# Performance work log

Hardware: AMD Instinct MI355X
Metric: run time of the kernel (lower is better)

Reference implementation:

```python
import jax, jax.numpy as jnp
import numpy as np

BITS = 4
GROUP = 128
IN = 4096
OUT = 14336
B = 64
PACK = 32 // BITS          # 8 values per int32
MAXQ = (1 << BITS) - 1     # 15


def setup_inputs() -> dict:
    key = jax.random.key(0)
    k = jax.random.split(key, 5)
    x = jax.random.normal(k[0], (B, IN), dtype=jnp.float32)
    # non-negative int32 so arithmetic right-shift behaves like logical shift
    qweight = jax.random.randint(k[1], (IN // PACK, OUT), 0, 2**31 - 1, dtype=jnp.int32)
    qzeros = jax.random.randint(k[2], (IN // GROUP, OUT // PACK), 0, 2**31 - 1, dtype=jnp.int32)
    scales = jax.random.uniform(k[3], (IN // GROUP, OUT), dtype=jnp.float32,
                                minval=1e-3, maxval=1e-2)
    bias = jax.random.normal(k[4], (OUT,), dtype=jnp.float32) * 0.01
    g_idx = (jnp.arange(IN) // GROUP).astype(jnp.int32)
    return dict(x=x, qweight=qweight, qzeros=qzeros, scales=scales, bias=bias, g_idx=g_idx)


def _dequant(qweight, qzeros, scales, g_idx):
    shifts = jnp.arange(PACK, dtype=jnp.int32) * BITS  # [PACK]
    # unpack weights: [IN//PACK, PACK, OUT] -> [IN, OUT]
    w = (qweight[:, None, :] >> shifts[None, :, None]) & MAXQ
    w = w.reshape(IN, OUT)
    # unpack zeros: [G, OUT//PACK, PACK] -> [G, OUT]; pack() stored (zeros-1), so add 1 back
    z = (qzeros[:, :, None] >> shifts[None, None, :]) & MAXQ
    z = z.reshape(-1, OUT) + 1
    # per-group dequant with arbitrary g_idx (act-order support)
    return scales[g_idx] * (w - z[g_idx]).astype(scales.dtype)


def reference(x, qweight, qzeros, scales, bias, g_idx):
    W = _dequant(qweight, qzeros, scales, g_idx)  # [IN, OUT]
    return x @ W + bias
```

## Files before the change

### kernel.cpp

```cpp
#include <hip/hip_runtime.h>
#include <hip/hip_bf16.h>

using u32 = unsigned int;
using u16 = unsigned short;

typedef __attribute__((ext_vector_type(8))) _Float16 half8;
typedef __attribute__((ext_vector_type(2))) _Float16 half2v;
typedef __attribute__((ext_vector_type(16))) float f32x16;
typedef __attribute__((ext_vector_type(4))) u32 u32x4;

#define IN_K   4096
#define OUT_N  14336
#define SPLITK 8
#define OUT_ELEMS (64 * OUT_N)

__global__ __launch_bounds__(256) void prep_kernel(const float* __restrict__ x,
                                                   u16* __restrict__ xs) {
  const int t = blockIdx.x * 256 + threadIdx.x;
  const int c = t >> 6;
  const int r = t & 63;
  const float* px = x + r * IN_K + c * 8;
  const float4 a = *(const float4*)px;
  const float4 b = *(const float4*)(px + 4);
  const float af[4] = {a.x, a.y, a.z, a.w};
  const float bf[4] = {b.x, b.y, b.z, b.w};
  union { u32x4 v; u32 u[4]; } o;
#pragma unroll
  for (int i = 0; i < 4; ++i) {
    const _Float16 hl = (_Float16)af[i];
    const _Float16 hh = (_Float16)bf[i];
    u16 lo, hi;
    __builtin_memcpy(&lo, &hl, 2);
    __builtin_memcpy(&hi, &hh, 2);
    o.u[i] = (u32)lo | ((u32)hi << 16);
  }
  *(u32x4*)(xs + (size_t)t * 8) = o.v;
}

__global__ __launch_bounds__(256) void bias_init_kernel(const float* __restrict__ bias,
                                                        float* __restrict__ out) {
  const int i = (blockIdx.x * 256 + threadIdx.x) * 4;
  const int col = i % OUT_N;
  *(float4*)(out + i) = *(const float4*)(bias + col);
}

__global__ __launch_bounds__(256) void reduce_kernel(const float* __restrict__ part,
                                                     const float* __restrict__ bias,
                                                     float* __restrict__ out) {
  const int gx = blockIdx.x, ry = blockIdx.y, t = threadIdx.x;
  const int bx = gx >> 1, half = gx & 1;
  const int row = ry * 8 + (t >> 5);
  const int cin = half * 128 + (t & 31) * 4;
  const float* p = part + (((size_t)bx * SPLITK) * 64 + row) * 256 + cin;
  float4 r = *(const float4*)(bias + bx * 256 + cin);
#pragma unroll
  for (int by = 0; by < SPLITK; ++by) {
    const float4 a = *(const float4*)(p + (size_t)by * 64 * 256);
    r.x += a.x; r.y += a.y; r.z += a.z; r.w += a.w;
  }
  *(float4*)(out + (size_t)row * OUT_N + bx * 256 + cin) = r;
}

static __device__ __forceinline__ half8 dequant8(u32 q, half2v hz, half2v s2) {
  const u32 p0 = (q & 0x000F000Fu) | 0x64006400u;
  const u32 p1 = ((q >> 4) & 0x000F000Fu) | 0x64006400u;
  const u32 p2 = ((q >> 8) & 0x000F000Fu) | 0x64006400u;
  const u32 p3 = ((q >> 12) & 0x000F000Fu) | 0x64006400u;
  half2v t0, t1, t2, t3;
  __builtin_memcpy(&t0, &p0, 4);
  __builtin_memcpy(&t1, &p1, 4);
  __builtin_memcpy(&t2, &p2, 4);
  __builtin_memcpy(&t3, &p3, 4);
  union { half8 v; half2v h[4]; } bb;
  bb.h[0] = (t0 - hz) * s2;
  bb.h[1] = (t1 - hz) * s2;
  bb.h[2] = (t2 - hz) * s2;
  bb.h[3] = (t3 - hz) * s2;
  return bb.v;
}

template <bool ATOMIC>
__global__ __launch_bounds__(512, 4) void qgemm_kernel(
    const u32* __restrict__ qw, const u32* __restrict__ qz,
    const float* __restrict__ scal, const u16* __restrict__ xs,
    float* __restrict__ dst) {
  __shared__ u16 alds[64 * 512];
  const int tid = threadIdx.x;
  const int lane = tid & 63;
  const int wv = tid >> 6;
  const int g = lane >> 5;
  const int nn = lane & 31;
  const int bx = blockIdx.x;
  const int by = blockIdx.y;
  const int colabs = bx * 256 + wv * 32 + nn;
  const int chunk0 = by * 64;
  const int grp0 = by * 4;
  const int zsh = (nn & 7) * 4;

  f32x16 acc0, acc1;
#pragma unroll
  for (int i = 0; i < 16; ++i) { acc0[i] = 0.f; acc1[i] = 0.f; }

  const u16* asrc = xs + (size_t)chunk0 * 512;
#pragma unroll
  for (int r = 0; r < 8; ++r) {
    const int p = r * 512 + tid;
    __builtin_amdgcn_global_load_lds(
        (const __attribute__((address_space(1))) void*)(asrc + p * 8),
        (__attribute__((address_space(3))) void*)(&alds[0] + p * 8), 16, 0, 0);
  }

  const u32* pq = qw + (size_t)(chunk0 + g) * OUT_N + colabs;
  u32 qv[32];
#pragma unroll
  for (int i = 0; i < 32; ++i) qv[i] = pq[(size_t)(2 * i) * OUT_N];

  float sv[4]; u32 zv[4];
#pragma unroll
  for (int t = 0; t < 4; ++t) {
    sv[t] = scal[(size_t)(grp0 + t) * OUT_N + colabs];
    zv[t] = qz[(size_t)(grp0 + t) * (OUT_N / 8) + (colabs >> 3)];
  }

  asm volatile("s_waitcnt vmcnt(0)" ::: "memory");
  __builtin_amdgcn_s_barrier();
  asm volatile("" ::: "memory");

#pragma unroll
  for (int grp = 0; grp < 4; ++grp) {
    const u32 zq = (zv[grp] >> zsh) & 0xFu;
    const u32 hzu = 0x64016401u + zq * 0x00010001u;
    half2v hz; __builtin_memcpy(&hz, &hzu, 4);
    const _Float16 hs = (_Float16)sv[grp];
    const half2v s2 = {hs, hs};
#pragma unroll
    for (int s = 0; s < 8; ++s) {
      const int t = grp * 8 + s;
      const int cl = 2 * t + g;
      const half8 a0 = *(const half8*)(&alds[0] + ((size_t)cl * 64 + nn) * 8);
      const half8 a1 = *(const half8*)(&alds[0] + ((size_t)cl * 64 + nn + 32) * 8);
      const half8 bb = dequant8(qv[t], hz, s2);
      acc0 = __builtin_amdgcn_mfma_f32_32x32x16_f16(a0, bb, acc0, 0, 0, 0);
      acc1 = __builtin_amdgcn_mfma_f32_32x32x16_f16(a1, bb, acc1, 0, 0, 0);
    }
  }

  if (ATOMIC) {
#pragma unroll
    for (int r = 0; r < 16; ++r) {
      const int row = (r & 3) + 8 * (r >> 2) + 4 * g;
      unsafeAtomicAdd(&dst[(size_t)row * OUT_N + colabs], acc0[r]);
      unsafeAtomicAdd(&dst[(size_t)(row + 32) * OUT_N + colabs], acc1[r]);
    }
  } else {
    float* p = dst + (((size_t)bx * SPLITK + by) * 64) * 256 + wv * 32 + nn;
#pragma unroll
    for (int r = 0; r < 16; ++r) {
      const int row = (r & 3) + 8 * (r >> 2) + 4 * g;
      p[(size_t)row * 256] = acc0[r];
      p[(size_t)(row + 32) * 256] = acc1[r];
    }
  }
}

extern "C" void kernel_launch(void* const* d_in, const int* in_sizes, int n_in,
                              void* d_out, int out_size, void* d_ws, size_t ws_size,
                              hipStream_t stream) {
  (void)in_sizes; (void)n_in; (void)out_size;
  const float* x    = (const float*)d_in[0];
  const u32*   qw   = (const u32*)d_in[1];
  const u32*   qz   = (const u32*)d_in[2];
  const float* sc   = (const float*)d_in[3];
  const float* bias = (const float*)d_in[4];
  float* out = (float*)d_out;

  const size_t XS_BYTES   = (size_t)64 * IN_K * 2;
  const size_t PART_BYTES = (size_t)56 * SPLITK * 64 * 256 * 4;
  u16* xs = (u16*)d_ws;

  prep_kernel<<<128, 256, 0, stream>>>(x, xs);

  if (ws_size >= XS_BYTES + PART_BYTES) {
    float* part = (float*)((char*)d_ws + XS_BYTES);
    qgemm_kernel<false><<<dim3(56, SPLITK), 512, 0, stream>>>(qw, qz, sc, xs, part);
    reduce_kernel<<<dim3(112, 8), 256, 0, stream>>>(part, bias, out);
  } else {
    bias_init_kernel<<<896, 256, 0, stream>>>(bias, out);
    qgemm_kernel<true><<<dim3(56, SPLITK), 512, 0, stream>>>(qw, qz, sc, xs, out);
  }
}
```

Baseline: 32.35 us.

## Move split-K reduction into block with double-buffered LDS pipeline, drop reduce kernel

Replaces the 56x8 split-K grid plus separate reduce kernel with 224 blocks that each cover 64 output columns. The four wave pairs in a block each take a quarter of K and combine their partial sums through shared memory in the epilogue, which also adds the bias. Activations and packed weights are streamed through double-buffered LDS using global_load_lds, with waitcnt and barriers so loads overlap the MFMA work. This removes the partials buffer round trip through global memory and one kernel launch. In exchange each block uses 80KB of LDS, needs many barriers, and the grid is smaller.

Result: faster. 26.36 us (-18.5%).

```diff
diff --git a/kernel.cpp b/kernel.cpp
--- a/kernel.cpp
+++ b/kernel.cpp
@@ -11,8 +11,7 @@
 
 #define IN_K   4096
 #define OUT_N  14336
-#define SPLITK 8
-#define OUT_ELEMS (64 * OUT_N)
+#define NST    16
 
 __global__ __launch_bounds__(256) void prep_kernel(const float* __restrict__ x,
                                                    u16* __restrict__ xs) {
@@ -37,30 +36,6 @@
   *(u32x4*)(xs + (size_t)t * 8) = o.v;
 }
 
-__global__ __launch_bounds__(256) void bias_init_kernel(const float* __restrict__ bias,
-                                                        float* __restrict__ out) {
-  const int i = (blockIdx.x * 256 + threadIdx.x) * 4;
-  const int col = i % OUT_N;
-  *(float4*)(out + i) = *(const float4*)(bias + col);
-}
-
-__global__ __launch_bounds__(256) void reduce_kernel(const float* __restrict__ part,
-                                                     const float* __restrict__ bias,
-                                                     float* __restrict__ out) {
-  const int gx = blockIdx.x, ry = blockIdx.y, t = threadIdx.x;
-  const int bx = gx >> 1, half = gx & 1;
-  const int row = ry * 8 + (t >> 5);
-  const int cin = half * 128 + (t & 31) * 4;
-  const float* p = part + (((size_t)bx * SPLITK) * 64 + row) * 256 + cin;
-  float4 r = *(const float4*)(bias + bx * 256 + cin);
-#pragma unroll
-  for (int by = 0; by < SPLITK; ++by) {
-    const float4 a = *(const float4*)(p + (size_t)by * 64 * 256);
-    r.x += a.x; r.y += a.y; r.z += a.z; r.w += a.w;
-  }
-  *(float4*)(out + (size_t)row * OUT_N + bx * 256 + cin) = r;
-}
-
 static __device__ __forceinline__ half8 dequant8(u32 q, half2v hz, half2v s2) {
   const u32 p0 = (q & 0x000F000Fu) | 0x64006400u;
   const u32 p1 = ((q >> 4) & 0x000F000Fu) | 0x64006400u;
@@ -79,113 +54,135 @@
   return bb.v;
 }
 
-template <bool ATOMIC>
 __global__ __launch_bounds__(512, 4) void qgemm_kernel(
     const u32* __restrict__ qw, const u32* __restrict__ qz,
     const float* __restrict__ scal, const u16* __restrict__ xs,
-    float* __restrict__ dst) {
-  __shared__ u16 alds[64 * 512];
+    const float* __restrict__ bias, float* __restrict__ out) {
+  __shared__ alignas(16) char smem[81920];
   const int tid = threadIdx.x;
   const int lane = tid & 63;
-  const int wv = tid >> 6;
   const int g = lane >> 5;
   const int nn = lane & 31;
+  const int wv = tid >> 6;
+  const int ch = wv & 1;
+  const int kq = wv >> 1;
+  const int tq = tid & 127;
   const int bx = blockIdx.x;
-  const int by = blockIdx.y;
-  const int colabs = bx * 256 + wv * 32 + nn;
-  const int chunk0 = by * 64;
-  const int grp0 = by * 4;
+  const int colabs = bx * 64 + ch * 32 + nn;
   const int zsh = (nn & 7) * 4;
+  char* const base = smem + kq * 20480;
 
   f32x16 acc0, acc1;
 #pragma unroll
   for (int i = 0; i < 16; ++i) { acc0[i] = 0.f; acc1[i] = 0.f; }
 
-  const u16* asrc = xs + (size_t)chunk0 * 512;
+  float sv[8]; u32 zv[8];
 #pragma unroll
-  for (int r = 0; r < 8; ++r) {
-    const int p = r * 512 + tid;
+  for (int t = 0; t < 8; ++t) {
+    sv[t] = scal[(size_t)(kq * 8 + t) * OUT_N + colabs];
+    zv[t] = qz[(size_t)(kq * 8 + t) * (OUT_N / 8) + (colabs >> 3)];
+  }
+  asm volatile("s_waitcnt vmcnt(0)" ::: "memory");
+
+  auto issue = [&](int st) {
+    const int slot = st & 1;
+    char* ab = base + slot * 8192;
+    char* qb = base + 16384 + slot * 2048;
+    const u16* asrc = xs + (size_t)(kq * 128 + st * 8) * 512;
+#pragma unroll
+    for (int r = 0; r < 4; ++r) {
+      const int p = r * 128 + tq;
+      __builtin_amdgcn_global_load_lds(
+          (const __attribute__((address_space(1))) void*)(asrc + p * 8),
+          (__attribute__((address_space(3))) void*)(ab + p * 16), 16, 0, 0);
+    }
+    const int j = tq >> 4, cg = tq & 15;
+    const u32* qsrc = qw + (size_t)(kq * 128 + st * 8 + j) * OUT_N
+                         + bx * 64 + cg * 4;
     __builtin_amdgcn_global_load_lds(
-        (const __attribute__((address_space(1))) void*)(asrc + p * 8),
-        (__attribute__((address_space(3))) void*)(&alds[0] + p * 8), 16, 0, 0);
-  }
+        (const __attribute__((address_space(1))) void*)qsrc,
+        (__attribute__((address_space(3))) void*)(qb + tq * 16), 16, 0, 0);
+  };
 
-  const u32* pq = qw + (size_t)(chunk0 + g) * OUT_N + colabs;
-  u32 qv[32];
-#pragma unroll
-  for (int i = 0; i < 32; ++i) qv[i] = pq[(size_t)(2 * i) * OUT_N];
-
-  float sv[4]; u32 zv[4];
-#pragma unroll
-  for (int t = 0; t < 4; ++t) {
-    sv[t] = scal[(size_t)(grp0 + t) * OUT_N + colabs];
-    zv[t] = qz[(size_t)(grp0 + t) * (OUT_N / 8) + (colabs >> 3)];
-  }
-
-  asm volatile("s_waitcnt vmcnt(0)" ::: "memory");
-  __builtin_amdgcn_s_barrier();
-  asm volatile("" ::: "memory");
+  issue(0); issue(1);
 
 #pragma unroll
-  for (int grp = 0; grp < 4; ++grp) {
-    const u32 zq = (zv[grp] >> zsh) & 0xFu;
+  for (int st = 0; st < NST; ++st) {
+    if (st < NST - 1)
+      asm volatile("s_waitcnt vmcnt(5)" ::: "memory");
+    else
+      asm volatile("s_waitcnt vmcnt(0)" ::: "memory");
+    __builtin_amdgcn_s_barrier();
+    asm volatile("" ::: "memory");
+
+    const int gi = st >> 1;
+    const u32 zq = (zv[gi] >> zsh) & 0xFu;
     const u32 hzu = 0x64016401u + zq * 0x00010001u;
     half2v hz; __builtin_memcpy(&hz, &hzu, 4);
-    const _Float16 hs = (_Float16)sv[grp];
+    const _Float16 hs = (_Float16)sv[gi];
     const half2v s2 = {hs, hs};
+
+    const u16* ab = (const u16*)(base + (st & 1) * 8192);
+    const u32* qb = (const u32*)(base + 16384 + (st & 1) * 2048);
+    __builtin_amdgcn_s_setprio(1);
 #pragma unroll
-    for (int s = 0; s < 8; ++s) {
-      const int t = grp * 8 + s;
-      const int cl = 2 * t + g;
-      const half8 a0 = *(const half8*)(&alds[0] + ((size_t)cl * 64 + nn) * 8);
-      const half8 a1 = *(const half8*)(&alds[0] + ((size_t)cl * 64 + nn + 32) * 8);
-      const half8 bb = dequant8(qv[t], hz, s2);
+    for (int s = 0; s < 4; ++s) {
+      const int cl = s * 2 + g;
+      const half8 a0 = *(const half8*)(ab + (cl * 64 + nn) * 8);
+      const half8 a1 = *(const half8*)(ab + (cl * 64 + nn + 32) * 8);
+      const u32 q = qb[cl * 64 + ch * 32 + nn];
+      const half8 bb = dequant8(q, hz, s2);
       acc0 = __builtin_amdgcn_mfma_f32_32x32x16_f16(a0, bb, acc0, 0, 0, 0);
       acc1 = __builtin_amdgcn_mfma_f32_32x32x16_f16(a1, bb, acc1, 0, 0, 0);
     }
+    __builtin_amdgcn_s_setprio(0);
+
+    if (st + 2 < NST) {
+      __builtin_amdgcn_s_barrier();
+      asm volatile("" ::: "memory");
+      issue(st + 2);
+    }
   }
 
-  if (ATOMIC) {
+  __syncthreads();
+  float* ep = (float*)smem + kq * 4096;
 #pragma unroll
-    for (int r = 0; r < 16; ++r) {
-      const int row = (r & 3) + 8 * (r >> 2) + 4 * g;
-      unsafeAtomicAdd(&dst[(size_t)row * OUT_N + colabs], acc0[r]);
-      unsafeAtomicAdd(&dst[(size_t)(row + 32) * OUT_N + colabs], acc1[r]);
-    }
-  } else {
-    float* p = dst + (((size_t)bx * SPLITK + by) * 64) * 256 + wv * 32 + nn;
+  for (int r = 0; r < 16; ++r) {
+    const int row0 = (r & 3) + 8 * (r >> 2) + 4 * g;
+    ep[row0 * 64 + ch * 32 + nn] = acc0[r];
+    ep[(row0 + 32) * 64 + ch * 32 + nn] = acc1[r];
+  }
+  __syncthreads();
+  const int pos = tid * 8;
+  const int row = pos >> 6;
+  const int colb = pos & 63;
+  const float* eb = (const float*)smem;
+  float4 v0 = *(const float4*)(bias + bx * 64 + colb);
+  float4 v1 = *(const float4*)(bias + bx * 64 + colb + 4);
 #pragma unroll
-    for (int r = 0; r < 16; ++r) {
-      const int row = (r & 3) + 8 * (r >> 2) + 4 * g;
-      p[(size_t)row * 256] = acc0[r];
-      p[(size_t)(row + 32) * 256] = acc1[r];
-    }
+  for (int q = 0; q < 4; ++q) {
+    const float4 a = *(const float4*)(eb + q * 4096 + pos);
+    const float4 b = *(const float4*)(eb + q * 4096 + pos + 4);
+    v0.x += a.x; v0.y += a.y; v0.z += a.z; v0.w += a.w;
+    v1.x += b.x; v1.y += b.y; v1.z += b.z; v1.w += b.w;
   }
+  float* po = out + (size_t)row * OUT_N + bx * 64 + colb;
+  *(float4*)po = v0;
+  *(float4*)(po + 4) = v1;
 }
 
 extern "C" void kernel_launch(void* const* d_in, const int* in_sizes, int n_in,
                               void* d_out, int out_size, void* d_ws, size_t ws_size,
                               hipStream_t stream) {
-  (void)in_sizes; (void)n_in; (void)out_size;
+  (void)in_sizes; (void)n_in; (void)out_size; (void)ws_size;
   const float* x    = (const float*)d_in[0];
   const u32*   qw   = (const u32*)d_in[1];
   const u32*   qz   = (const u32*)d_in[2];
   const float* sc   = (const float*)d_in[3];
   const float* bias = (const float*)d_in[4];
   float* out = (float*)d_out;
-
-  const size_t XS_BYTES   = (size_t)64 * IN_K * 2;
-  const size_t PART_BYTES = (size_t)56 * SPLITK * 64 * 256 * 4;
   u16* xs = (u16*)d_ws;
 
   prep_kernel<<<128, 256, 0, stream>>>(x, xs);
-
-  if (ws_size >= XS_BYTES + PART_BYTES) {
-    float* part = (float*)((char*)d_ws + XS_BYTES);
-    qgemm_kernel<false><<<dim3(56, SPLITK), 512, 0, stream>>>(qw, qz, sc, xs, part);
-    reduce_kernel<<<dim3(112, 8), 256, 0, stream>>>(part, bias, out);
-  } else {
-    bias_init_kernel<<<896, 256, 0, stream>>>(bias, out);
-    qgemm_kernel<true><<<dim3(56, SPLITK), 512, 0, stream>>>(qw, qz, sc, xs, out);
-  }
+  qgemm_kernel<<<224, 512, 0, stream>>>(qw, qz, sc, xs, bias, out);
 }
```
